# Kernel optimization log

Hardware: AMD Instinct MI355X
Metric: run time of the kernel (lower is better)

Reference implementation:

```python
import jax, jax.numpy as jnp
import numpy as np

TOP_K = 2  # matches init top_k


def setup_inputs() -> dict:
    key = jax.random.key(0)
    k = jax.random.split(key, 5)
    B, S, D, E, H = 8, 2048, 768, 8, 3072  # batch, seq, n_embed, num_experts, 4*n_embed
    init = lambda kk, shape: (jax.random.normal(kk, shape, jnp.float32) * 0.02)
    return {
        "x": jax.random.normal(k[0], (B, S, D), jnp.float32),
        "Wg": init(k[1], (D, E)),            # router weight
        "bg": jnp.zeros((E,), jnp.float32),   # router bias
        "W1": init(k[2], (E, D, H)),          # stacked expert fc1
        "b1": jnp.zeros((E, H), jnp.float32),
        "W2": init(k[3], (E, H, D)),          # stacked expert fc2
        "b2": jnp.zeros((E, D), jnp.float32),
    }


def _moe(x, Wg, bg, W1, b1, W2, b2):
    B, S, D = x.shape
    E = Wg.shape[1]
    # --- TopkRouter: top-k logits, softmax over selected experts, scatter to full gate tensor ---
    logits = x @ Wg + bg                                  # [B,S,E]
    top_vals, top_idx = jax.lax.top_k(logits, TOP_K)      # [B,S,K]
    gates_k = jax.nn.softmax(top_vals, axis=-1)           # softmax over the k selected experts only
    one_hot = jax.nn.one_hot(top_idx, E, dtype=x.dtype)   # [B,S,K,E] (E is small)
    gates = jnp.sum(one_hot * gates_k[..., None], axis=-2)  # [B,S,E], zeros off top-k

    # --- dispatch/compute/combine: scan over experts (fixed, small), gate-weighted accumulate ---
    flat_x = x.reshape(-1, D)          # [T,D]
    flat_g = gates.reshape(-1, E).T    # [E,T]

    def body(acc, p):
        W1e, b1e, W2e, b2e, ge = p
        h = jax.nn.relu(flat_x @ W1e + b1e)               # [T,H]
        acc = acc + (h @ W2e + b2e) * ge[:, None]         # gate==0 -> zero contribution (incl. bias)
        return acc, None

    out, _ = jax.lax.scan(body, jnp.zeros_like(flat_x), (W1, b1, W2, b2, flat_g))
    return out.reshape(B, S, D)


def reference(x, Wg, bg, W1, b1, W2, b2):
    return _moe(x, Wg, bg, W1, b1, W2, b2)
```

## Files before the change

kernel.cpp:

```cpp
#include <hip/hip_runtime.h>
#include <stdint.h>

typedef unsigned short u16;
typedef __attribute__((ext_vector_type(8))) short v8s;
typedef __attribute__((ext_vector_type(4))) float v4f;

#define T_TOK 16384
#define DIM   768
#define NE    8
#define HH    3072
#define MCAP  34816
#define GM    (MCAP/256)

#define O_W1T 0u
#define O_W2T 37748736u
#define O_XBF 75497472u
#define O_STK 100663296u
#define O_SGT 100802560u
#define O_TE  100941824u
#define O_TG  101072896u
#define O_TS  101203968u
#define O_MET 101335040u
#define O_HBF 101335296u
#define HBF_A2 213909504u
#define HBF_A  106954752u
#define OBF_SZ 53477376u
#define WS_TIER_A2 (O_HBF + HBF_A2 + OBF_SZ)
#define WS_TIER_A  (O_HBF + HBF_A  + OBF_SZ)

__device__ __forceinline__ u16 f2bf(float f){
  uint32_t u = __float_as_uint(f);
  uint32_t r = (u + 0x7fffu + ((u >> 16) & 1u)) >> 16;
  return (u16)r;
}
__device__ __forceinline__ float bf2f(u16 v){
  return __uint_as_float(((uint32_t)v) << 16);
}
__device__ __forceinline__ void gll16(const u16* g, u16* l){
  __builtin_amdgcn_global_load_lds((const __attribute__((address_space(1))) uint32_t*)g,
                                   (__attribute__((address_space(3))) uint32_t*)l, 16, 0, 0);
}

#define BAR() do { asm volatile("" ::: "memory"); __builtin_amdgcn_s_barrier(); asm volatile("" ::: "memory"); } while(0)
#define WAIT_LGKM0() asm volatile("s_waitcnt lgkmcnt(0)" ::: "memory")
#define WAIT_VM4() asm volatile("s_waitcnt vmcnt(4)" ::: "memory")
#define WAIT_VM0() asm volatile("s_waitcnt vmcnt(0)" ::: "memory")

__global__ void k_transposeW1(const float* __restrict__ W1, u16* __restrict__ W1t){
  __shared__ float tile[32][33];
  int e = blockIdx.z;
  int h0 = blockIdx.x * 32, d0 = blockIdx.y * 32;
  const float* src = W1 + (size_t)e * DIM * HH;
  u16* dst = W1t + (size_t)e * HH * DIM;
  int tx = threadIdx.x, ty = threadIdx.y;
  #pragma unroll
  for (int j = 0; j < 4; j++)
    tile[ty + 8*j][tx] = src[(size_t)(d0 + ty + 8*j) * HH + h0 + tx];
  __syncthreads();
  #pragma unroll
  for (int j = 0; j < 4; j++)
    dst[(size_t)(h0 + ty + 8*j) * DIM + d0 + tx] = f2bf(tile[tx][ty + 8*j]);
}

__global__ void k_transposeW2(const float* __restrict__ W2, u16* __restrict__ W2t){
  __shared__ float tile[32][33];
  int e = blockIdx.z;
  int d0 = blockIdx.x * 32, h0 = blockIdx.y * 32;
  const float* src = W2 + (size_t)e * HH * DIM;
  u16* dst = W2t + (size_t)e * DIM * HH;
  int tx = threadIdx.x, ty = threadIdx.y;
  #pragma unroll
  for (int j = 0; j < 4; j++)
    tile[ty + 8*j][tx] = src[(size_t)(h0 + ty + 8*j) * DIM + d0 + tx];
  __syncthreads();
  #pragma unroll
  for (int j = 0; j < 4; j++)
    dst[(size_t)(d0 + ty + 8*j) * HH + h0 + tx] = f2bf(tile[tx][ty + 8*j]);
}

__global__ __launch_bounds__(256) void k_router(
    const float* __restrict__ x, const float* __restrict__ Wg, const float* __restrict__ bg,
    int* __restrict__ tE, float* __restrict__ tG, u16* __restrict__ Xbf){
  int t = blockIdx.x * 4 + (threadIdx.x >> 6);
  int l = threadIdx.x & 63;
  const float* xr = x + (size_t)t * DIM;
  u16* xb = Xbf + (size_t)t * DIM;
  float acc[NE];
  #pragma unroll
  for (int e = 0; e < NE; e++) acc[e] = 0.f;
  #pragma unroll
  for (int j = 0; j < DIM / 64; j++){
    int c = l + 64 * j;
    float xv = xr[c];
    xb[c] = f2bf(xv);
    const float4* wr4 = (const float4*)(Wg + (size_t)c * NE);
    float4 w0 = wr4[0], w1 = wr4[1];
    acc[0] += xv * w0.x; acc[1] += xv * w0.y; acc[2] += xv * w0.z; acc[3] += xv * w0.w;
    acc[4] += xv * w1.x; acc[5] += xv * w1.y; acc[6] += xv * w1.z; acc[7] += xv * w1.w;
  }
  #pragma unroll
  for (int off = 32; off; off >>= 1)
    #pragma unroll
    for (int e = 0; e < NE; e++) acc[e] += __shfl_xor(acc[e], off, 64);

  if (l == 0){
    float lgt[NE];
    #pragma unroll
    for (int e = 0; e < NE; e++) lgt[e] = acc[e] + bg[e];
    int i0 = 0; float v0 = lgt[0];
    #pragma unroll
    for (int e = 1; e < NE; e++) if (lgt[e] > v0){ v0 = lgt[e]; i0 = e; }
    int i1 = -1; float v1 = -1e30f;
    #pragma unroll
    for (int e = 0; e < NE; e++) if (e != i0 && lgt[e] > v1){ v1 = lgt[e]; i1 = e; }
    float ed = expf(v1 - v0);
    float g1 = ed / (1.f + ed);
    float g0 = 1.f / (1.f + ed);
    tE[2*t] = i0; tE[2*t+1] = i1;
    tG[2*t] = g0; tG[2*t+1] = g1;
  }
}

__global__ __launch_bounds__(256) void k_count(const int* __restrict__ tE, int* __restrict__ counts){
  int i = blockIdx.x * blockDim.x + threadIdx.x;
  int c[NE];
  #pragma unroll
  for (int e = 0; e < NE; e++) c[e] = 0;
  for (int j = i; j < 2 * T_TOK; j += 32 * 256){
    int v = tE[j];
    #pragma unroll
    for (int e = 0; e < NE; e++) c[e] += (v == e);
  }
  #pragma unroll
  for (int off = 32; off; off >>= 1)
    #pragma unroll
    for (int e = 0; e < NE; e++) c[e] += __shfl_xor(c[e], off, 64);
  if ((threadIdx.x & 63) == 0){
    #pragma unroll
    for (int e = 0; e < NE; e++) atomicAdd(&counts[e], c[e]);
  }
}

__global__ void k_scan(const int* __restrict__ counts, int* __restrict__ offs){
  if (threadIdx.x == 0){
    int o = 0;
    for (int e = 0; e < NE; e++){ offs[e] = o; o += (counts[e] + 255) & ~255; }
    offs[NE] = o;
  }
}

__global__ __launch_bounds__(256) void k_scatter(
    const int* __restrict__ tE, const float* __restrict__ tG,
    const int* __restrict__ offs, int* __restrict__ fill,
    int* __restrict__ slot_token, float* __restrict__ slot_gate, int* __restrict__ tSlot){
  int t = blockIdx.x * 256 + threadIdx.x;
  int lane = threadIdx.x & 63, w = threadIdx.x >> 6;
  int e0 = tE[2*t], e1 = tE[2*t+1];
  float g0 = tG[2*t], g1 = tG[2*t+1];

  __shared__ int wcnt[4][NE];
  __shared__ int woff[4][NE];
  __shared__ int bbase[NE];

  uint64_t below = (1ull << lane) - 1ull;
  int rank0 = 0, rank1 = 0;
  #pragma unroll
  for (int e = 0; e < NE; e++){
    uint64_t m0 = __ballot(e0 == e);
    uint64_t m1 = __ballot(e1 == e);
    int c0 = __popcll(m0);
    if (e0 == e) rank0 = __popcll(m0 & below);
    if (e1 == e) rank1 = c0 + __popcll(m1 & below);
    if (lane == 0) wcnt[w][e] = c0 + __popcll(m1);
  }
  __syncthreads();
  if (threadIdx.x < NE){
    int e = threadIdx.x;
    int s = 0;
    #pragma unroll
    for (int ww = 0; ww < 4; ww++){ woff[ww][e] = s; s += wcnt[ww][e]; }
    bbase[e] = atomicAdd(&fill[e], s);
  }
  __syncthreads();
  int p0 = offs[e0] + bbase[e0] + woff[w][e0] + rank0;
  slot_token[p0] = t; slot_gate[p0] = g0; tSlot[2*t] = p0;
  int p1 = offs[e1] + bbase[e1] + woff[w][e1] + rank1;
  slot_token[p1] = t; slot_gate[p1] = g1; tSlot[2*t+1] = p1;
}

__global__ void k_outinit(const int* __restrict__ tE, const float* __restrict__ tG,
                          const float* __restrict__ b2, float* __restrict__ out){
  int t = blockIdx.x;
  int e0 = tE[2*t], e1 = tE[2*t+1];
  float g0 = tG[2*t], g1 = tG[2*t+1];
  const float* r0 = b2 + (size_t)e0 * DIM;
  const float* r1 = b2 + (size_t)e1 * DIM;
  float* o = out + (size_t)t * DIM;
  #pragma unroll
  for (int j = 0; j < DIM / 256; j++){
    int c = threadIdx.x + 256 * j;
    o[c] = g0 * r0[c] + g1 * r1[c];
  }
}


#define ABASE(b,h) (((b)*2+(h))*8192)
#define BBASE(b,h) (32768 + ((b)*2+(h))*8192)
#define SWZE(ro,ks) (((((ro)*128) + (ks)*64 + lg*16) ^ (((lm)&7)<<4)) >> 1)

#define STAGE2(p0, p1, base, kk) do { \
  gll16((p0) + (kk), &lds[(base) + (w*2)*512]); \
  gll16((p1) + (kk), &lds[(base) + (w*2+1)*512]); } while(0)

#define MFMA_Q(MOFF, NOFF, BF) \
  __builtin_amdgcn_s_setprio(1); \
  _Pragma("unroll") \
  for (int mi = 0; mi < 4; mi++) \
    _Pragma("unroll") \
    for (int ni = 0; ni < 2; ni++) \
      _Pragma("unroll") \
      for (int ks = 0; ks < 2; ks++) \
        acc[(MOFF)+mi][(NOFF)+ni] = __builtin_amdgcn_mfma_f32_16x16x32_bf16(aF[mi][ks], BF[ni][ks], acc[(MOFF)+mi][(NOFF)+ni], 0, 0, 0); \
  __builtin_amdgcn_s_setprio(0);

__device__ __forceinline__ int find_expert(const int* offs, int grb, int& total){
  int offr[NE+1];
  #pragma unroll
  for (int i = 0; i <= NE; i++) offr[i] = offs[i];
  total = offr[NE];
  int e = 0;
  #pragma unroll
  for (int i = 1; i < NE; i++) e += (grb >= offr[i]);
  return e;
}

__global__ __launch_bounds__(512, 2) void k_gemm1(
    const u16* __restrict__ Xbf, const u16* __restrict__ W1t, const float* __restrict__ b1,
    const int* __restrict__ slot_token, const float* __restrict__ slot_gate,
    const int* __restrict__ offs, u16* __restrict__ Hbuf, int hs, int cbase, int ntc)
{
  int bid = blockIdx.x;
  int swz = (bid & 7) * ((int)gridDim.x >> 3) + (bid >> 3);
  int mt = swz / ntc, ntile = swz % ntc;
  int grb = mt * 256;
  int total;
  int e = find_expert(offs, grb, total);
  if (grb >= total) return;
  int nb = ntile * 256;
  int habs = cbase + nb;

  __shared__ __align__(16) u16 lds[65536];

  int tid = threadIdx.x, w = tid >> 6, lane = tid & 63;
  int wm = w >> 2, wn = w & 3, lm = lane & 15, lg = lane >> 4;
  int cbe = (((lane & 7) ^ (lane >> 3)) << 3);

  int rA00 = (w*2+0)*8 + (lane>>3), rA01 = (w*2+1)*8 + (lane>>3);
  const u16 *sA00 = Xbf + (size_t)slot_token[grb + rA00]       * DIM + cbe;
  const u16 *sA01 = Xbf + (size_t)slot_token[grb + rA01]       * DIM + cbe;
  const u16 *sA10 = Xbf + (size_t)slot_token[grb + 128 + rA00] * DIM + cbe;
  const u16 *sA11 = Xbf + (size_t)slot_token[grb + 128 + rA01] * DIM + cbe;
  const u16 *sB00 = W1t + ((size_t)e*HH + habs + rA00)       * DIM + cbe;
  const u16 *sB01 = W1t + ((size_t)e*HH + habs + rA01)       * DIM + cbe;
  const u16 *sB10 = W1t + ((size_t)e*HH + habs + 128 + rA00) * DIM + cbe;
  const u16 *sB11 = W1t + ((size_t)e*HH + habs + 128 + rA01) * DIM + cbe;

  v4f acc[8][4];
  #pragma unroll
  for (int mi = 0; mi < 8; mi++)
    #pragma unroll
    for (int ni = 0; ni < 4; ni++) acc[mi][ni] = 0.f;

  const int NTK = DIM / 64;
  STAGE2(sA00, sA01, ABASE(0,0), 0);  STAGE2(sA10, sA11, ABASE(0,1), 0);
  STAGE2(sB00, sB01, BBASE(0,0), 0);  STAGE2(sB10, sB11, BBASE(0,1), 0);
  STAGE2(sA00, sA01, ABASE(1,0), 64); STAGE2(sA10, sA11, ABASE(1,1), 64);
  WAIT_VM4(); BAR();

  v8s aF[4][2], bF0[2][2], bF1[2][2];
  for (int k = 0; k < NTK; ++k){
    int cur = k & 1, nx = cur ^ 1;
    int ab = ABASE(cur, wm);
    int bb = BBASE(cur, wn >> 1);
    #pragma unroll
    for (int mi = 0; mi < 4; mi++)
      #pragma unroll
      for (int ks = 0; ks < 2; ks++)
        aF[mi][ks] = *(const v8s*)&lds[ab + SWZE(mi*16 + lm, ks)];
    #pragma unroll
    for (int ni = 0; ni < 2; ni++)
      #pragma unroll
      for (int ks = 0; ks < 2; ks++)
        bF0[ni][ks] = *(const v8s*)&lds[bb + SWZE((wn&1)*64 + ni*16 + lm, ks)];
    if (k + 1 < NTK) STAGE2(sB00, sB01, BBASE(nx,0), (k+1)*64);
    MFMA_Q(0, 0, bF0);
    BAR();
    #pragma unroll
    for (int ni = 0; ni < 2; ni++)
      #pragma unroll
      for (int ks = 0; ks < 2; ks++)
        bF1[ni][ks] = *(const v8s*)&lds[bb + SWZE((wn&1)*64 + (2+ni)*16 + lm, ks)];
    if (k + 1 < NTK) STAGE2(sB10, sB11, BBASE(nx,1), (k+1)*64);
    MFMA_Q(0, 2, bF1);
    BAR();
    #pragma unroll
    for (int mi = 0; mi < 4; mi++)
      #pragma unroll
      for (int ks = 0; ks < 2; ks++)
        aF[mi][ks] = *(const v8s*)&lds[ab + SWZE((4+mi)*16 + lm, ks)];
    MFMA_Q(4, 0, bF0);
    WAIT_LGKM0(); BAR();
    if (k + 2 < NTK){
      STAGE2(sA00, sA01, ABASE(cur,0), (k+2)*64);
      STAGE2(sA10, sA11, ABASE(cur,1), (k+2)*64);
    }
    MFMA_Q(4, 2, bF1);
    if (k + 2 < NTK) { WAIT_VM4(); } else { WAIT_VM0(); }
    BAR();
  }

  float b1v[4];
  #pragma unroll
  for (int ni = 0; ni < 4; ni++) b1v[ni] = b1[(size_t)e * HH + habs + wn*64 + ni*16 + lm];
  #pragma unroll
  for (int mi = 0; mi < 8; mi++){
    int rbase = grb + wm*128 + mi*16 + lg*4;
    float g[4];
    #pragma unroll
    for (int i = 0; i < 4; i++) g[i] = slot_gate[rbase + i];
    #pragma unroll
    for (int ni = 0; ni < 4; ni++){
      int col = nb + wn*64 + ni*16 + lm;
      #pragma unroll
      for (int i = 0; i < 4; i++){
        float v = acc[mi][ni][i] + b1v[ni];
        v = fmaxf(v, 0.f) * g[i];
        Hbuf[(size_t)(rbase + i) * hs + col] = f2bf(v);
      }
    }
  }
}

__global__ __launch_bounds__(512, 2) void k_gemm2(
    const u16* __restrict__ Hbuf, const u16* __restrict__ W2t,
    const int* __restrict__ slot_token, const int* __restrict__ offs,
    float* __restrict__ out, u16* __restrict__ Obuf, int hs, int cbase, int klen, int mode)
{
  const int NT = DIM / 256;
  int bid = blockIdx.x;
  int swz = (bid & 7) * ((int)gridDim.x >> 3) + (bid >> 3);
  int mt = swz / NT, ntile = swz % NT;
  int grb = mt * 256;
  int total;
  int e = find_expert(offs, grb, total);
  if (grb >= total) return;
  int nb = ntile * 256;

  __shared__ __align__(16) u16 lds[65536];

  int tid = threadIdx.x, w = tid >> 6, lane = tid & 63;
  int wm = w >> 2, wn = w & 3, lm = lane & 15, lg = lane >> 4;
  int cbe = (((lane & 7) ^ (lane >> 3)) << 3);

  int rA00 = (w*2+0)*8 + (lane>>3), rA01 = (w*2+1)*8 + (lane>>3);
  const u16 *sA00 = Hbuf + (size_t)(grb + rA00)       * hs + cbe;
  const u16 *sA01 = Hbuf + (size_t)(grb + rA01)       * hs + cbe;
  const u16 *sA10 = Hbuf + (size_t)(grb + 128 + rA00) * hs + cbe;
  const u16 *sA11 = Hbuf + (size_t)(grb + 128 + rA01) * hs + cbe;
  const u16 *sB00 = W2t + ((size_t)e*DIM + nb + rA00)       * HH + cbase + cbe;
  const u16 *sB01 = W2t + ((size_t)e*DIM + nb + rA01)       * HH + cbase + cbe;
  const u16 *sB10 = W2t + ((size_t)e*DIM + nb + 128 + rA00) * HH + cbase + cbe;
  const u16 *sB11 = W2t + ((size_t)e*DIM + nb + 128 + rA01) * HH + cbase + cbe;

  v4f acc[8][4];
  #pragma unroll
  for (int mi = 0; mi < 8; mi++)
    #pragma unroll
    for (int ni = 0; ni < 4; ni++) acc[mi][ni] = 0.f;

  const int ntk = klen / 64;
  STAGE2(sA00, sA01, ABASE(0,0), 0);  STAGE2(sA10, sA11, ABASE(0,1), 0);
  STAGE2(sB00, sB01, BBASE(0,0), 0);  STAGE2(sB10, sB11, BBASE(0,1), 0);
  STAGE2(sA00, sA01, ABASE(1,0), 64); STAGE2(sA10, sA11, ABASE(1,1), 64);
  WAIT_VM4(); BAR();

  v8s aF[4][2], bF0[2][2], bF1[2][2];
  for (int k = 0; k < ntk; ++k){
    int cur = k & 1, nx = cur ^ 1;
    int ab = ABASE(cur, wm);
    int bb = BBASE(cur, wn >> 1);
    #pragma unroll
    for (int mi = 0; mi < 4; mi++)
      #pragma unroll
      for (int ks = 0; ks < 2; ks++)
        aF[mi][ks] = *(const v8s*)&lds[ab + SWZE(mi*16 + lm, ks)];
    #pragma unroll
    for (int ni = 0; ni < 2; ni++)
      #pragma unroll
      for (int ks = 0; ks < 2; ks++)
        bF0[ni][ks] = *(const v8s*)&lds[bb + SWZE((wn&1)*64 + ni*16 + lm, ks)];
    if (k + 1 < ntk) STAGE2(sB00, sB01, BBASE(nx,0), (k+1)*64);
    MFMA_Q(0, 0, bF0);
    BAR();
    #pragma unroll
    for (int ni = 0; ni < 2; ni++)
      #pragma unroll
      for (int ks = 0; ks < 2; ks++)
        bF1[ni][ks] = *(const v8s*)&lds[bb + SWZE((wn&1)*64 + (2+ni)*16 + lm, ks)];
    if (k + 1 < ntk) STAGE2(sB10, sB11, BBASE(nx,1), (k+1)*64);
    MFMA_Q(0, 2, bF1);
    BAR();
    #pragma unroll
    for (int mi = 0; mi < 4; mi++)
      #pragma unroll
      for (int ks = 0; ks < 2; ks++)
        aF[mi][ks] = *(const v8s*)&lds[ab + SWZE((4+mi)*16 + lm, ks)];
    MFMA_Q(4, 0, bF0);
    WAIT_LGKM0(); BAR();
    if (k + 2 < ntk){
      STAGE2(sA00, sA01, ABASE(cur,0), (k+2)*64);
      STAGE2(sA10, sA11, ABASE(cur,1), (k+2)*64);
    }
    MFMA_Q(4, 2, bF1);
    if (k + 2 < ntk) { WAIT_VM4(); } else { WAIT_VM0(); }
    BAR();
  }

  if (mode == 0){
    #pragma unroll
    for (int mi = 0; mi < 8; mi++){
      int rbase = grb + wm*128 + mi*16 + lg*4;
      int tok[4];
      #pragma unroll
      for (int i = 0; i < 4; i++) tok[i] = slot_token[rbase + i];
      #pragma unroll
      for (int ni = 0; ni < 4; ni++){
        int col = nb + wn*64 + ni*16 + lm;
        #pragma unroll
        for (int i = 0; i < 4; i++)
          unsafeAtomicAdd(&out[(size_t)tok[i] * DIM + col], acc[mi][ni][i]);
      }
    }
  } else if (mode == 1){
    #pragma unroll
    for (int mi = 0; mi < 8; mi++){
      int rbase = grb + wm*128 + mi*16 + lg*4;
      #pragma unroll
      for (int ni = 0; ni < 4; ni++){
        int col = nb + wn*64 + ni*16 + lm;
        #pragma unroll
        for (int i = 0; i < 4; i++)
          Obuf[(size_t)(rbase + i) * DIM + col] = f2bf(acc[mi][ni][i]);
      }
    }
  } else {
    #pragma unroll
    for (int mi = 0; mi < 8; mi++){
      int rbase = grb + wm*128 + mi*16 + lg*4;
      #pragma unroll
      for (int ni = 0; ni < 4; ni++){
        int col = nb + wn*64 + ni*16 + lm;
        #pragma unroll
        for (int i = 0; i < 4; i++){
          size_t p = (size_t)(rbase + i) * DIM + col;
          Obuf[p] = f2bf(bf2f(Obuf[p]) + acc[mi][ni][i]);
        }
      }
    }
  }
}

__global__ __launch_bounds__(192) void k_combine(
    const u16* __restrict__ Obuf, const int* __restrict__ tSlot,
    const int* __restrict__ tE, const float* __restrict__ tG,
    const float* __restrict__ b2, float* __restrict__ out)
{
  int t = blockIdx.x;
  int l = threadIdx.x;
  int s0 = tSlot[2*t], s1 = tSlot[2*t+1];
  int e0 = tE[2*t], e1 = tE[2*t+1];
  float g0 = tG[2*t], g1 = tG[2*t+1];
  int c = l * 4;
  ushort4 a = *(const ushort4*)(Obuf + (size_t)s0 * DIM + c);
  ushort4 b = *(const ushort4*)(Obuf + (size_t)s1 * DIM + c);
  float4 bA = *(const float4*)(b2 + (size_t)e0 * DIM + c);
  float4 bB = *(const float4*)(b2 + (size_t)e1 * DIM + c);
  float4 r;
  r.x = bf2f(a.x) + bf2f(b.x) + g0 * bA.x + g1 * bB.x;
  r.y = bf2f(a.y) + bf2f(b.y) + g0 * bA.y + g1 * bB.y;
  r.z = bf2f(a.z) + bf2f(b.z) + g0 * bA.z + g1 * bB.z;
  r.w = bf2f(a.w) + bf2f(b.w) + g0 * bA.w + g1 * bB.w;
  *(float4*)(out + (size_t)t * DIM + c) = r;
}

extern "C" void kernel_launch(void* const* d_in, const int* in_sizes, int n_in,
                              void* d_out, int out_size, void* d_ws, size_t ws_size,
                              hipStream_t stream)
{
  const float* x  = (const float*)d_in[0];
  const float* Wg = (const float*)d_in[1];
  const float* bg = (const float*)d_in[2];
  const float* W1 = (const float*)d_in[3];
  const float* b1 = (const float*)d_in[4];
  const float* W2 = (const float*)d_in[5];
  const float* b2 = (const float*)d_in[6];
  float* out = (float*)d_out;
  char* ws = (char*)d_ws;

  u16*   W1t        = (u16*)(ws + O_W1T);
  u16*   W2t        = (u16*)(ws + O_W2T);
  u16*   Xbf        = (u16*)(ws + O_XBF);
  u16*   Hbuf       = (u16*)(ws + O_HBF);
  int*   slot_token = (int*)(ws + O_STK);
  float* slot_gate  = (float*)(ws + O_SGT);
  int*   tE         = (int*)(ws + O_TE);
  float* tG         = (float*)(ws + O_TG);
  int*   tSlot      = (int*)(ws + O_TS);
  int*   meta       = (int*)(ws + O_MET);
  int*   counts = meta;
  int*   fill   = meta + 8;
  int*   offs   = meta + 16;

  const int tier = (ws_size >= WS_TIER_A2) ? 2 : (ws_size >= WS_TIER_A) ? 1 : 0;
  const unsigned hbf_sz = (tier == 2) ? HBF_A2 : HBF_A;
  u16* Obuf = (u16*)(ws + O_HBF + hbf_sz);

  hipMemsetAsync(ws + O_STK, 0, O_TE - O_STK, stream);
  hipMemsetAsync(ws + O_MET, 0, 128, stream);

  k_transposeW1<<<dim3(HH/32, DIM/32, NE), dim3(32, 8), 0, stream>>>(W1, W1t);
  k_transposeW2<<<dim3(DIM/32, HH/32, NE), dim3(32, 8), 0, stream>>>(W2, W2t);

  k_router<<<T_TOK/4, 256, 0, stream>>>(x, Wg, bg, tE, tG, Xbf);
  k_count<<<32, 256, 0, stream>>>(tE, counts);
  k_scan<<<1, 1, 0, stream>>>(counts, offs);
  k_scatter<<<T_TOK/256, 256, 0, stream>>>(tE, tG, offs, fill, slot_token, slot_gate, tSlot);
  if (tier == 0)
    k_outinit<<<T_TOK, 256, 0, stream>>>(tE, tG, b2, out);

  if (tier == 2){
    k_gemm1<<<GM * (HH/256), 512, 0, stream>>>(Xbf, W1t, b1, slot_token, slot_gate, offs, Hbuf, HH, 0, HH/256);
    k_gemm2<<<GM * (DIM/256), 512, 0, stream>>>(Hbuf, W2t, slot_token, offs, out, Obuf, HH, 0, HH, 1);
    k_combine<<<T_TOK, 192, 0, stream>>>(Obuf, tSlot, tE, tG, b2, out);
  } else {
    const int CH = 1536;
    for (int c = 0; c < 2; c++){
      k_gemm1<<<GM * (CH/256), 512, 0, stream>>>(Xbf, W1t, b1, slot_token, slot_gate, offs, Hbuf, CH, c*CH, CH/256);
      int mode = (tier == 1) ? (c == 0 ? 1 : 2) : 0;
      k_gemm2<<<GM * (DIM/256), 512, 0, stream>>>(Hbuf, W2t, slot_token, offs, out, Obuf, CH, c*CH, CH, mode);
    }
    if (tier == 1)
      k_combine<<<T_TOK, 192, 0, stream>>>(Obuf, tSlot, tE, tG, b2, out);
  }
}
```

Baseline: 492.6 us.

## Drop bf16 Obuf/combine pass, scatter GEMM2 via atomics, vectorize transposes and router

Removes the intermediate bf16 Obuf and the k_combine kernel. GEMM2 now always atomically adds fp32 results into the output, which is pre-initialized with gated biases by k_outinit. This saves the Obuf write/read round trip and one launch, at the cost of scattered fp32 atomics to global memory. The weight transpose kernels are merged into one generic 64x64-tile kernel with float4 loads and ushort4 stores, and the router uses float4 loads and vectorized bf16 writes.

```diff
diff --git a/kernel.cpp b/kernel.cpp
--- a/kernel.cpp
+++ b/kernel.cpp
@@ -19,23 +19,16 @@
 #define O_SGT 100802560u
 #define O_TE  100941824u
 #define O_TG  101072896u
-#define O_TS  101203968u
 #define O_MET 101335040u
 #define O_HBF 101335296u
 #define HBF_A2 213909504u
-#define HBF_A  106954752u
-#define OBF_SZ 53477376u
-#define WS_TIER_A2 (O_HBF + HBF_A2 + OBF_SZ)
-#define WS_TIER_A  (O_HBF + HBF_A  + OBF_SZ)
+#define WS_FULLK (O_HBF + HBF_A2)
 
 __device__ __forceinline__ u16 f2bf(float f){
   uint32_t u = __float_as_uint(f);
   uint32_t r = (u + 0x7fffu + ((u >> 16) & 1u)) >> 16;
   return (u16)r;
 }
-__device__ __forceinline__ float bf2f(u16 v){
-  return __uint_as_float(((uint32_t)v) << 16);
-}
 __device__ __forceinline__ void gll16(const u16* g, u16* l){
   __builtin_amdgcn_global_load_lds((const __attribute__((address_space(1))) uint32_t*)g,
                                    (__attribute__((address_space(3))) uint32_t*)l, 16, 0, 0);
@@ -46,36 +39,31 @@
 #define WAIT_VM4() asm volatile("s_waitcnt vmcnt(4)" ::: "memory")
 #define WAIT_VM0() asm volatile("s_waitcnt vmcnt(0)" ::: "memory")
 
-__global__ void k_transposeW1(const float* __restrict__ W1, u16* __restrict__ W1t){
-  __shared__ float tile[32][33];
+__global__ __launch_bounds__(256) void k_transpose(
+    const float* __restrict__ src, u16* __restrict__ dst, int R, int C){
+  __shared__ float tile[64][65];
   int e = blockIdx.z;
-  int h0 = blockIdx.x * 32, d0 = blockIdx.y * 32;
-  const float* src = W1 + (size_t)e * DIM * HH;
-  u16* dst = W1t + (size_t)e * HH * DIM;
+  int c0 = blockIdx.x * 64, r0 = blockIdx.y * 64;
+  const float* s = src + (size_t)e * R * C;
+  u16* d = dst + (size_t)e * R * C;
   int tx = threadIdx.x, ty = threadIdx.y;
   #pragma unroll
-  for (int j = 0; j < 4; j++)
-    tile[ty + 8*j][tx] = src[(size_t)(d0 + ty + 8*j) * HH + h0 + tx];
+  for (int j = 0; j < 4; j++){
+    float4 v = *(const float4*)&s[(size_t)(r0 + ty + 16*j) * C + c0 + tx*4];
+    tile[ty+16*j][tx*4+0] = v.x; tile[ty+16*j][tx*4+1] = v.y;
+    tile[ty+16*j][tx*4+2] = v.z; tile[ty+16*j][tx*4+3] = v.w;
+  }
   __syncthreads();
   #pragma unroll
-  for (int j = 0; j < 4; j++)
-    dst[(size_t)(h0 + ty + 8*j) * DIM + d0 + tx] = f2bf(tile[tx][ty + 8*j]);
-}
-
-__global__ void k_transposeW2(const float* __restrict__ W2, u16* __restrict__ W2t){
-  __shared__ float tile[32][33];
-  int e = blockIdx.z;
-  int d0 = blockIdx.x * 32, h0 = blockIdx.y * 32;
-  const float* src = W2 + (size_t)e * HH * DIM;
-  u16* dst = W2t + (size_t)e * DIM * HH;
-  int tx = threadIdx.x, ty = threadIdx.y;
-  #pragma unroll
-  for (int j = 0; j < 4; j++)
-    tile[ty + 8*j][tx] = src[(size_t)(h0 + ty + 8*j) * DIM + d0 + tx];
-  __syncthreads();
-  #pragma unroll
-  for (int j = 0; j < 4; j++)
-    dst[(size_t)(d0 + ty + 8*j) * HH + h0 + tx] = f2bf(tile[tx][ty + 8*j]);
+  for (int j = 0; j < 4; j++){
+    int cc = ty + 16*j;
+    ushort4 o;
+    o.x = f2bf(tile[tx*4+0][cc]);
+    o.y = f2bf(tile[tx*4+1][cc]);
+    o.z = f2bf(tile[tx*4+2][cc]);
+    o.w = f2bf(tile[tx*4+3][cc]);
+    *(ushort4*)&d[(size_t)(c0 + cc) * R + r0 + tx*4] = o;
+  }
 }
 
 __global__ __launch_bounds__(256) void k_router(
@@ -83,20 +71,25 @@
     int* __restrict__ tE, float* __restrict__ tG, u16* __restrict__ Xbf){
   int t = blockIdx.x * 4 + (threadIdx.x >> 6);
   int l = threadIdx.x & 63;
-  const float* xr = x + (size_t)t * DIM;
-  u16* xb = Xbf + (size_t)t * DIM;
+  const float4* xr4 = (const float4*)(x + (size_t)t * DIM);
+  ushort4* xb4 = (ushort4*)(Xbf + (size_t)t * DIM);
   float acc[NE];
   #pragma unroll
   for (int e = 0; e < NE; e++) acc[e] = 0.f;
   #pragma unroll
-  for (int j = 0; j < DIM / 64; j++){
-    int c = l + 64 * j;
-    float xv = xr[c];
-    xb[c] = f2bf(xv);
-    const float4* wr4 = (const float4*)(Wg + (size_t)c * NE);
-    float4 w0 = wr4[0], w1 = wr4[1];
-    acc[0] += xv * w0.x; acc[1] += xv * w0.y; acc[2] += xv * w0.z; acc[3] += xv * w0.w;
-    acc[4] += xv * w1.x; acc[5] += xv * w1.y; acc[6] += xv * w1.z; acc[7] += xv * w1.w;
+  for (int j = 0; j < DIM / 256; j++){
+    int c4 = l + 64 * j;
+    float4 xv = xr4[c4];
+    ushort4 o; o.x = f2bf(xv.x); o.y = f2bf(xv.y); o.z = f2bf(xv.z); o.w = f2bf(xv.w);
+    xb4[c4] = o;
+    float xs[4] = {xv.x, xv.y, xv.z, xv.w};
+    #pragma unroll
+    for (int q = 0; q < 4; q++){
+      const float4* wr4 = (const float4*)(Wg + (size_t)(4*c4 + q) * NE);
+      float4 w0 = wr4[0], w1 = wr4[1];
+      acc[0] += xs[q]*w0.x; acc[1] += xs[q]*w0.y; acc[2] += xs[q]*w0.z; acc[3] += xs[q]*w0.w;
+      acc[4] += xs[q]*w1.x; acc[5] += xs[q]*w1.y; acc[6] += xs[q]*w1.z; acc[7] += xs[q]*w1.w;
+    }
   }
   #pragma unroll
   for (int off = 32; off; off >>= 1)
@@ -152,7 +145,7 @@
 __global__ __launch_bounds__(256) void k_scatter(
     const int* __restrict__ tE, const float* __restrict__ tG,
     const int* __restrict__ offs, int* __restrict__ fill,
-    int* __restrict__ slot_token, float* __restrict__ slot_gate, int* __restrict__ tSlot){
+    int* __restrict__ slot_token, float* __restrict__ slot_gate){
   int t = blockIdx.x * 256 + threadIdx.x;
   int lane = threadIdx.x & 63, w = threadIdx.x >> 6;
   int e0 = tE[2*t], e1 = tE[2*t+1];
@@ -183,9 +176,9 @@
   }
   __syncthreads();
   int p0 = offs[e0] + bbase[e0] + woff[w][e0] + rank0;
-  slot_token[p0] = t; slot_gate[p0] = g0; tSlot[2*t] = p0;
+  slot_token[p0] = t; slot_gate[p0] = g0;
   int p1 = offs[e1] + bbase[e1] + woff[w][e1] + rank1;
-  slot_token[p1] = t; slot_gate[p1] = g1; tSlot[2*t+1] = p1;
+  slot_token[p1] = t; slot_gate[p1] = g1;
 }
 
 __global__ void k_outinit(const int* __restrict__ tE, const float* __restrict__ tG,
@@ -344,7 +337,7 @@
 __global__ __launch_bounds__(512, 2) void k_gemm2(
     const u16* __restrict__ Hbuf, const u16* __restrict__ W2t,
     const int* __restrict__ slot_token, const int* __restrict__ offs,
-    float* __restrict__ out, u16* __restrict__ Obuf, int hs, int cbase, int klen, int mode)
+    float* __restrict__ out, int hs, int cbase, int klen)
 {
   const int NT = DIM / 256;
   int bid = blockIdx.x;
@@ -426,71 +419,20 @@
     BAR();
   }
 
-  if (mode == 0){
-    #pragma unroll
-    for (int mi = 0; mi < 8; mi++){
-      int rbase = grb + wm*128 + mi*16 + lg*4;
-      int tok[4];
-      #pragma unroll
-      for (int i = 0; i < 4; i++) tok[i] = slot_token[rbase + i];
-      #pragma unroll
-      for (int ni = 0; ni < 4; ni++){
-        int col = nb + wn*64 + ni*16 + lm;
-        #pragma unroll
-        for (int i = 0; i < 4; i++)
-          unsafeAtomicAdd(&out[(size_t)tok[i] * DIM + col], acc[mi][ni][i]);
-      }
-    }
-  } else if (mode == 1){
-    #pragma unroll
-    for (int mi = 0; mi < 8; mi++){
-      int rbase = grb + wm*128 + mi*16 + lg*4;
-      #pragma unroll
-      for (int ni = 0; ni < 4; ni++){
-        int col = nb + wn*64 + ni*16 + lm;
-        #pragma unroll
-        for (int i = 0; i < 4; i++)
-          Obuf[(size_t)(rbase + i) * DIM + col] = f2bf(acc[mi][ni][i]);
-      }
-    }
-  } else {
-    #pragma unroll
-    for (int mi = 0; mi < 8; mi++){
-      int rbase = grb + wm*128 + mi*16 + lg*4;
-      #pragma unroll
-      for (int ni = 0; ni < 4; ni++){
-        int col = nb + wn*64 + ni*16 + lm;
-        #pragma unroll
-        for (int i = 0; i < 4; i++){
-          size_t p = (size_t)(rbase + i) * DIM + col;
-          Obuf[p] = f2bf(bf2f(Obuf[p]) + acc[mi][ni][i]);
-        }
-      }
-    }
-  }
-}
-
-__global__ __launch_bounds__(192) void k_combine(
-    const u16* __restrict__ Obuf, const int* __restrict__ tSlot,
-    const int* __restrict__ tE, const float* __restrict__ tG,
-    const float* __restrict__ b2, float* __restrict__ out)
-{
-  int t = blockIdx.x;
-  int l = threadIdx.x;
-  int s0 = tSlot[2*t], s1 = tSlot[2*t+1];
-  int e0 = tE[2*t], e1 = tE[2*t+1];
-  float g0 = tG[2*t], g1 = tG[2*t+1];
-  int c = l * 4;
-  ushort4 a = *(const ushort4*)(Obuf + (size_t)s0 * DIM + c);
-  ushort4 b = *(const ushort4*)(Obuf + (size_t)s1 * DIM + c);
-  float4 bA = *(const float4*)(b2 + (size_t)e0 * DIM + c);
-  float4 bB = *(const float4*)(b2 + (size_t)e1 * DIM + c);
-  float4 r;
-  r.x = bf2f(a.x) + bf2f(b.x) + g0 * bA.x + g1 * bB.x;
-  r.y = bf2f(a.y) + bf2f(b.y) + g0 * bA.y + g1 * bB.y;
-  r.z = bf2f(a.z) + bf2f(b.z) + g0 * bA.z + g1 * bB.z;
-  r.w = bf2f(a.w) + bf2f(b.w) + g0 * bA.w + g1 * bB.w;
-  *(float4*)(out + (size_t)t * DIM + c) = r;
+  #pragma unroll
+  for (int mi = 0; mi < 8; mi++){
+    int rbase = grb + wm*128 + mi*16 + lg*4;
+    int tok[4];
+    #pragma unroll
+    for (int i = 0; i < 4; i++) tok[i] = slot_token[rbase + i];
+    #pragma unroll
+    for (int ni = 0; ni < 4; ni++){
+      int col = nb + wn*64 + ni*16 + lm;
+      #pragma unroll
+      for (int i = 0; i < 4; i++)
+        unsafeAtomicAdd(&out[(size_t)tok[i] * DIM + col], acc[mi][ni][i]);
+    }
+  }
 }
 
 extern "C" void kernel_launch(void* const* d_in, const int* in_sizes, int n_in,
@@ -515,41 +457,33 @@
   float* slot_gate  = (float*)(ws + O_SGT);
   int*   tE         = (int*)(ws + O_TE);
   float* tG         = (float*)(ws + O_TG);
-  int*   tSlot      = (int*)(ws + O_TS);
   int*   meta       = (int*)(ws + O_MET);
   int*   counts = meta;
   int*   fill   = meta + 8;
   int*   offs   = meta + 16;
 
-  const int tier = (ws_size >= WS_TIER_A2) ? 2 : (ws_size >= WS_TIER_A) ? 1 : 0;
-  const unsigned hbf_sz = (tier == 2) ? HBF_A2 : HBF_A;
-  u16* Obuf = (u16*)(ws + O_HBF + hbf_sz);
+  const bool fullK = (ws_size >= WS_FULLK);
 
   hipMemsetAsync(ws + O_STK, 0, O_TE - O_STK, stream);
   hipMemsetAsync(ws + O_MET, 0, 128, stream);
 
-  k_transposeW1<<<dim3(HH/32, DIM/32, NE), dim3(32, 8), 0, stream>>>(W1, W1t);
-  k_transposeW2<<<dim3(DIM/32, HH/32, NE), dim3(32, 8), 0, stream>>>(W2, W2t);
+  k_transpose<<<dim3(HH/64, DIM/64, NE), dim3(16, 16), 0, stream>>>(W1, W1t, DIM, HH);
+  k_transpose<<<dim3(DIM/64, HH/64, NE), dim3(16, 16), 0, stream>>>(W2, W2t, HH, DIM);
 
   k_router<<<T_TOK/4, 256, 0, stream>>>(x, Wg, bg, tE, tG, Xbf);
   k_count<<<32, 256, 0, stream>>>(tE, counts);
   k_scan<<<1, 1, 0, stream>>>(counts, offs);
-  k_scatter<<<T_TOK/256, 256, 0, stream>>>(tE, tG, offs, fill, slot_token, slot_gate, tSlot);
-  if (tier == 0)
-    k_outinit<<<T_TOK, 256, 0, stream>>>(tE, tG, b2, out);
-
-  if (tier == 2){
+  k_scatter<<<T_TOK/256, 256, 0, stream>>>(tE, tG, offs, fill, slot_token, slot_gate);
+  k_outinit<<<T_TOK, 256, 0, stream>>>(tE, tG, b2, out);
+
+  if (fullK){
     k_gemm1<<<GM * (HH/256), 512, 0, stream>>>(Xbf, W1t, b1, slot_token, slot_gate, offs, Hbuf, HH, 0, HH/256);
-    k_gemm2<<<GM * (DIM/256), 512, 0, stream>>>(Hbuf, W2t, slot_token, offs, out, Obuf, HH, 0, HH, 1);
-    k_combine<<<T_TOK, 192, 0, stream>>>(Obuf, tSlot, tE, tG, b2, out);
+    k_gemm2<<<GM * (DIM/256), 512, 0, stream>>>(Hbuf, W2t, slot_token, offs, out, HH, 0, HH);
   } else {
     const int CH = 1536;
     for (int c = 0; c < 2; c++){
       k_gemm1<<<GM * (CH/256), 512, 0, stream>>>(Xbf, W1t, b1, slot_token, slot_gate, offs, Hbuf, CH, c*CH, CH/256);
-      int mode = (tier == 1) ? (c == 0 ? 1 : 2) : 0;
-      k_gemm2<<<GM * (DIM/256), 512, 0, stream>>>(Hbuf, W2t, slot_token, offs, out, Obuf, CH, c*CH, CH, mode);
-    }
-    if (tier == 1)
-      k_combine<<<T_TOK, 192, 0, stream>>>(Obuf, tSlot, tE, tG, b2, out);
-  }
-}
+      k_gemm2<<<GM * (DIM/256), 512, 0, stream>>>(Hbuf, W2t, slot_token, offs, out, CH, c*CH, CH);
+    }
+  }
+}
```

Result: slower. 847.2 us (+72.0%).
